# Performance work log

Hardware: AMD Instinct MI355X
Metric: run time of the kernel (lower is better)

The kernel has to match this reference:

```python
import jax, jax.numpy as jnp
import numpy as np

VOCAB = 256
UNITS = 512

def setup_inputs() -> dict:
    key = jax.random.key(0)
    ks = jax.random.split(key, 7)
    B, T = 64, 1024
    scale = 0.02
    return {
        "inputs": jax.random.randint(ks[0], (B, T), 0, VOCAB, dtype=jnp.int32),
        "emb": jax.random.normal(ks[1], (VOCAB, VOCAB), dtype=jnp.float32) * scale,
        "Wx": jax.random.normal(ks[2], (VOCAB, UNITS), dtype=jnp.float32) * scale,
        "Wh": jax.random.normal(ks[3], (UNITS, UNITS), dtype=jnp.float32) * scale,
        "b": jnp.zeros((UNITS,), dtype=jnp.float32),
        "Wd": jax.random.normal(ks[4], (UNITS, VOCAB), dtype=jnp.float32) * scale,
        "bd": jnp.zeros((VOCAB,), dtype=jnp.float32),
    }

def reference(inputs, emb, Wx, Wh, b, Wd, bd):
    # Embedding lookup: [B, T] -> [B, T, VOCAB]
    x = emb[inputs]
    B = x.shape[0]
    # Precompute input projection for all timesteps (one big GEMM)
    xp = jnp.einsum("bte,eu->btu", x, Wx) + b  # [B, T, U]
    h0 = jnp.zeros((B, Wh.shape[0]), dtype=x.dtype)

    def step(h, xp_t):
        h_new = jnp.tanh(xp_t + h @ Wh)  # SimpleRNN cell: tanh(x W_x + h W_h + b)
        return h_new, h_new

    _, hs = jax.lax.scan(step, h0, jnp.swapaxes(xp, 0, 1))  # hs: [T, B, U]
    hs = jnp.swapaxes(hs, 0, 1)  # [B, T, U]
    logits = jnp.einsum("btu,uv->btv", hs, Wd) + bd  # [B, T, VOCAB]
    return logits
```

## Files before the change

### kernel.cpp

```cpp
#include <hip/hip_runtime.h>
#include <math.h>

#define BB   64
#define TT_  1024
#define UU   512
#define VV   256
#define EE   256
#define TC   128

__device__ __forceinline__ float tanh_fast(float x) {
    float e = __expf(x + x);
    return 1.f - 2.f * __builtin_amdgcn_rcpf(e + 1.f);
}

__device__ __forceinline__ int swz(int a) {
    return a ^ (((a >> 3) & 7) ^ ((a >> 6) & 1));
}

__global__ __launch_bounds__(512) void e2_kernel(
    const float* __restrict__ emb, const float* __restrict__ Wx,
    const float* __restrict__ bias, float* __restrict__ E2)
{
    const int v = blockIdx.x;
    const int u = threadIdx.x;
    float acc = bias[u];
    const float* er = emb + v * EE;
    #pragma unroll 8
    for (int e = 0; e < EE; ++e)
        acc = fmaf(er[e], Wx[e * UU + u], acc);
    E2[v * UU + u] = acc;
}

__global__ __launch_bounds__(512)
void rnn_chunk_kernel(
    const int* __restrict__ toks, const float* __restrict__ E2,
    const float* __restrict__ Wh, const float* __restrict__ Wd,
    const float* __restrict__ bd,
    unsigned long long* hpub,
    float* out, int t0, int last)
{
    __shared__ __align__(16) float hstage[2][2][UU];
    __shared__ __align__(16) float xps[2][2][64];
    __shared__ int stok[2][TC];

    const int bid  = blockIdx.x;
    const int bg   = bid & 31;
    const int ug   = bid >> 5;
    const int tid  = threadIdx.x;
    const int w    = tid >> 6;
    const int lane = tid & 63;
    const int b0   = bg * 2;

    const int qsel = lane >> 5;
    const int ks   = lane & 31;
    const int quad = w * 2 + qsel;
    const int fmv  = ((ks >> 1) & 7) ^ ((ks >> 4) & 1);
    const int v0   = ug * 32 + quad * 2;

    float4 whreg[16];
    {
        const float4* Wh4 = (const float4*)Wh;
        #pragma unroll
        for (int r = 0; r < 16; ++r)
            whreg[r] = Wh4[(ks * 16 + r) * 128 + ug * 16 + quad];
    }
    #pragma unroll
    for (int r = 0; r < 16; ++r) {
        float px = whreg[r].x, py = whreg[r].y, pz = whreg[r].z, pw = whreg[r].w;
        asm volatile("" : "+v"(px), "+v"(py), "+v"(pz), "+v"(pw));
        whreg[r] = make_float4(px, py, pz, pw);
    }

    float wdreg[32];
    #pragma unroll
    for (int j = 0; j < 16; ++j) {
        const float2 wd2 = *(const float2*)(Wd + (ks * 16 + j) * VV + v0);
        wdreg[j]      = wd2.x;
        wdreg[16 + j] = wd2.y;
    }
    const float bdv0 = bd[v0];
    const float bdv1 = bd[v0 + 1];

    if (tid < 256) {
        const int b = tid >> 7, q = tid & 127;
        stok[b][q] = toks[(b0 + b) * TT_ + t0 + q];
    }
    if (tid < 128) {
        const int b = tid >> 6, u = tid & 63;
        xps[0][b][u] = E2[toks[(b0 + b) * TT_ + t0] * UU + ug * 64 + u];
    }
    __syncthreads();

    for (int tt = 0; tt < TC; ++tt) {
        const int s  = t0 + tt;
        const int sl = (s - 1) & 1;

        if (s > 0 && (w != ug || tt == 0)) {
            unsigned long long* a0 = hpub + ((size_t)sl * BB + b0) * UU + w * 64 + lane;
            unsigned long long* a1 = a0 + UU;
            volatile const unsigned long long* f0 = a0;
            volatile const unsigned long long* f1 = a1;
            const unsigned int want = (unsigned int)(s - 1);
            unsigned long long p0 = 0, p1 = 0;
            bool got = false;
            for (int it = 0; it < 24; ++it) {
                p0 = *f0; p1 = *f1;
                unsigned long long ok =
                    __ballot((unsigned int)(p0 >> 32) == want) &
                    __ballot((unsigned int)(p1 >> 32) == want);
                if (ok == 0xFFFFFFFFFFFFFFFFull) { got = true; break; }
            }
            if (!got) {
                while (true) {
                    p0 = __hip_atomic_load(a0, __ATOMIC_RELAXED, __HIP_MEMORY_SCOPE_AGENT);
                    p1 = __hip_atomic_load(a1, __ATOMIC_RELAXED, __HIP_MEMORY_SCOPE_AGENT);
                    unsigned long long ok =
                        __ballot((unsigned int)(p0 >> 32) == want) &
                        __ballot((unsigned int)(p1 >> 32) == want);
                    if (ok == 0xFFFFFFFFFFFFFFFFull) break;
                    __builtin_amdgcn_s_sleep(1);
                }
            }
            const int aa = w * 16 + (lane >> 2);
            const int fi = swz(aa) * 4 + (lane & 3);
            hstage[sl][0][fi] = __uint_as_float((unsigned int)p0);
            hstage[sl][1][fi] = __uint_as_float((unsigned int)p1);
        }
        asm volatile("s_waitcnt lgkmcnt(0)" ::: "memory");
        __builtin_amdgcn_s_barrier();

        float xpre = 0.f;
        const bool dopre = (tid < 128) && (tt + 1 < TC);
        if (dopre)
            xpre = E2[stok[tid >> 6][tt + 1] * UU + ug * 64 + (tid & 63)];

        float acc0[4] = {0.f, 0.f, 0.f, 0.f};
        float acc1[4] = {0.f, 0.f, 0.f, 0.f};
        float hsv0[16], hsv1[16];
        if (s > 0) {
            const float* H0 = hstage[sl][0];
            const float* H1 = hstage[sl][1];
            #pragma unroll
            for (int g = 0; g < 4; ++g) {
                const int as2 = (4 * ks + g) ^ fmv;
                const float4 ha = *(const float4*)(H0 + as2 * 4);
                const float4 hc = *(const float4*)(H1 + as2 * 4);
                const float av[4] = {ha.x, ha.y, ha.z, ha.w};
                const float cv[4] = {hc.x, hc.y, hc.z, hc.w};
                #pragma unroll
                for (int m = 0; m < 4; ++m) {
                    hsv0[g * 4 + m] = av[m];
                    hsv1[g * 4 + m] = cv[m];
                    const float4 wv = whreg[g * 4 + m];
                    acc0[0] = fmaf(av[m], wv.x, acc0[0]);
                    acc0[1] = fmaf(av[m], wv.y, acc0[1]);
                    acc0[2] = fmaf(av[m], wv.z, acc0[2]);
                    acc0[3] = fmaf(av[m], wv.w, acc0[3]);
                    acc1[0] = fmaf(cv[m], wv.x, acc1[0]);
                    acc1[1] = fmaf(cv[m], wv.y, acc1[1]);
                    acc1[2] = fmaf(cv[m], wv.z, acc1[2]);
                    acc1[3] = fmaf(cv[m], wv.w, acc1[3]);
                }
            }
        }
        if (dopre)
            xps[(s + 1) & 1][tid >> 6][tid & 63] = xpre;

        float tba[4];
        #pragma unroll
        for (int c = 0; c < 4; ++c) {
            const float x = (ks & 16) ? acc0[c] : acc1[c];
            const float y = __shfl_xor(x, 16, 64);
            tba[c] = ((ks & 16) ? acc1[c] : acc0[c]) + y;
        }
        float ua, ub;
        {
            const float x0 = (ks & 8) ? tba[0] : tba[2];
            const float x1 = (ks & 8) ? tba[1] : tba[3];
            const float y0 = __shfl_xor(x0, 8, 64);
            const float y1 = __shfl_xor(x1, 8, 64);
            ua = ((ks & 8) ? tba[2] : tba[0]) + y0;
            ub = ((ks & 8) ? tba[3] : tba[1]) + y1;
        }
        float v;
        {
            const float x = (ks & 4) ? ua : ub;
            const float y = __shfl_xor(x, 4, 64);
            v = ((ks & 4) ? ub : ua) + y;
        }
        v += __shfl_xor(v, 1, 64);
        v += __shfl_xor(v, 2, 64);

        if ((ks & 3) == 0) {
            const int b = (ks >> 4) & 1;
            const int c = (((ks >> 3) & 1) << 1) | ((ks >> 2) & 1);
            const int u = quad * 4 + c;
            const float h = tanh_fast(v + xps[s & 1][b][u]);
            unsigned long long* dst =
                hpub + ((size_t)(s & 1) * BB + b0 + b) * UU + ug * 64 + u;
            const unsigned long long pk =
                ((unsigned long long)(unsigned int)s << 32) | __float_as_uint(h);
            *(volatile unsigned long long*)dst = pk;
            __hip_atomic_store(dst, pk, __ATOMIC_RELAXED, __HIP_MEMORY_SCOPE_AGENT);
            hstage[s & 1][b][swz(ug * 16 + quad) * 4 + c] = h;
        }

        if (s > 0) {
            float s00 = 0.f, s01 = 0.f, s10 = 0.f, s11 = 0.f;
            #pragma unroll
            for (int g = 0; g < 4; ++g) {
                #pragma unroll
                for (int m = 0; m < 4; ++m) {
                    s00 = fmaf(hsv0[g * 4 + m], wdreg[4 * g + m],      s00);
                    s01 = fmaf(hsv0[g * 4 + m], wdreg[16 + 4 * g + m], s01);
                    s10 = fmaf(hsv1[g * 4 + m], wdreg[4 * g + m],      s10);
                    s11 = fmaf(hsv1[g * 4 + m], wdreg[16 + 4 * g + m], s11);
                }
            }
            float pa, pb;
            {
                const float x0 = (ks & 16) ? s00 : s10;
                const float x1 = (ks & 16) ? s01 : s11;
                const float y0 = __shfl_xor(x0, 16, 64);
                const float y1 = __shfl_xor(x1, 16, 64);
                pa = ((ks & 16) ? s10 : s00) + y0;
                pb = ((ks & 16) ? s11 : s01) + y1;
            }
            float L;
            {
                const float x = (ks & 8) ? pa : pb;
                const float y = __shfl_xor(x, 8, 64);
                L = ((ks & 8) ? pb : pa) + y;
            }
            L += __shfl_xor(L, 1, 64);
            L += __shfl_xor(L, 2, 64);
            L += __shfl_xor(L, 4, 64);
            if ((ks & 7) == 0) {
                const int b    = (ks >> 4) & 1;
                const int voff = (ks >> 3) & 1;
                out[((size_t)(b0 + b) * TT_ + (s - 1)) * VV + v0 + voff]
                    = L + (voff ? bdv1 : bdv0);
            }
        }
    }

    if (last) {
        const int s  = t0 + TC - 1;
        const int sl = s & 1;
        if (w != ug) {
            unsigned long long* a0 = hpub + ((size_t)sl * BB + b0) * UU + w * 64 + lane;
            unsigned long long* a1 = a0 + UU;
            volatile const unsigned long long* f0 = a0;
            volatile const unsigned long long* f1 = a1;
            const unsigned int want = (unsigned int)s;
            unsigned long long p0 = 0, p1 = 0;
            bool got = false;
            for (int it = 0; it < 24; ++it) {
                p0 = *f0; p1 = *f1;
                unsigned long long ok =
                    __ballot((unsigned int)(p0 >> 32) == want) &
                    __ballot((unsigned int)(p1 >> 32) == want);
                if (ok == 0xFFFFFFFFFFFFFFFFull) { got = true; break; }
            }
            if (!got) {
                while (true) {
                    p0 = __hip_atomic_load(a0, __ATOMIC_RELAXED, __HIP_MEMORY_SCOPE_AGENT);
                    p1 = __hip_atomic_load(a1, __ATOMIC_RELAXED, __HIP_MEMORY_SCOPE_AGENT);
                    unsigned long long ok =
                        __ballot((unsigned int)(p0 >> 32) == want) &
                        __ballot((unsigned int)(p1 >> 32) == want);
                    if (ok == 0xFFFFFFFFFFFFFFFFull) break;
                    __builtin_amdgcn_s_sleep(1);
                }
            }
            const int aa = w * 16 + (lane >> 2);
            const int fi = swz(aa) * 4 + (lane & 3);
            hstage[sl][0][fi] = __uint_as_float((unsigned int)p0);
            hstage[sl][1][fi] = __uint_as_float((unsigned int)p1);
        }
        __syncthreads();
        {
            const float* H0 = hstage[sl][0];
            const float* H1 = hstage[sl][1];
            float s00 = 0.f, s01 = 0.f, s10 = 0.f, s11 = 0.f;
            #pragma unroll
            for (int g = 0; g < 4; ++g) {
                const int as2 = (4 * ks + g) ^ fmv;
                const float4 ha = *(const float4*)(H0 + as2 * 4);
                const float4 hc = *(const float4*)(H1 + as2 * 4);
                const float av[4] = {ha.x, ha.y, ha.z, ha.w};
                const float cv[4] = {hc.x, hc.y, hc.z, hc.w};
                #pragma unroll
                for (int m = 0; m < 4; ++m) {
                    s00 = fmaf(av[m], wdreg[4 * g + m],      s00);
                    s01 = fmaf(av[m], wdreg[16 + 4 * g + m], s01);
                    s10 = fmaf(cv[m], wdreg[4 * g + m],      s10);
                    s11 = fmaf(cv[m], wdreg[16 + 4 * g + m], s11);
                }
            }
            float pa, pb;
            {
                const float x0 = (ks & 16) ? s00 : s10;
                const float x1 = (ks & 16) ? s01 : s11;
                const float y0 = __shfl_xor(x0, 16, 64);
                const float y1 = __shfl_xor(x1, 16, 64);
                pa = ((ks & 16) ? s10 : s00) + y0;
                pb = ((ks & 16) ? s11 : s01) + y1;
            }
            float L;
            {
                const float x = (ks & 8) ? pa : pb;
                const float y = __shfl_xor(x, 8, 64);
                L = ((ks & 8) ? pb : pa) + y;
            }
            L += __shfl_xor(L, 1, 64);
            L += __shfl_xor(L, 2, 64);
            L += __shfl_xor(L, 4, 64);
            if ((ks & 7) == 0) {
                const int b    = (ks >> 4) & 1;
                const int voff = (ks >> 3) & 1;
                out[((size_t)(b0 + b) * TT_ + s) * VV + v0 + voff]
                    = L + (voff ? bdv1 : bdv0);
            }
        }
    }
}

extern "C" void kernel_launch(void* const* d_in, const int* in_sizes, int n_in,
                              void* d_out, int out_size, void* d_ws, size_t ws_size,
                              hipStream_t stream)
{
    (void)in_sizes; (void)n_in; (void)ws_size; (void)out_size;

    const int*   toks = (const int*)  d_in[0];
    const float* emb  = (const float*)d_in[1];
    const float* Wx   = (const float*)d_in[2];
    const float* Wh   = (const float*)d_in[3];
    const float* bias = (const float*)d_in[4];
    const float* Wd   = (const float*)d_in[5];
    const float* bd   = (const float*)d_in[6];
    float* out = (float*)d_out;

    unsigned long long* hpub = (unsigned long long*)d_ws;
    float* E2 = (float*)(hpub + 2 * BB * UU);

    hipMemsetAsync(hpub, 0xFF, (size_t)(2 * BB * UU) * sizeof(unsigned long long), stream);
    e2_kernel<<<EE, UU, 0, stream>>>(emb, Wx, bias, E2);

    for (int c = 0; c < TT_ / TC; ++c) {
        const int t0 = c * TC;
        rnn_chunk_kernel<<<256, 512, 0, stream>>>(
            toks, E2, Wh, Wd, bd, hpub, out, t0, c == (TT_ / TC - 1));
    }
}
```

Measured before the change: 2.272 ms.

## Prefetch next-step hidden-state flags before output GEMV and double time chunk

Each wave now issues a speculative load of the next step's published hidden-state slots right after computing its own tanh outputs. The load overlaps the output-projection work, and the prefetched value is checked before falling back to polling. The time chunk per block also grows from 128 to 256, and all threads now load the token chunk. The aim is to hide cross-block polling latency on the serial recurrence and to reduce per-chunk startup overhead, at the cost of more LDS for tokens and possibly fewer parallel blocks.

Result: slower. 3.255 ms (+43.3%).

```diff
diff --git a/kernel.cpp b/kernel.cpp
--- a/kernel.cpp
+++ b/kernel.cpp
@@ -6,7 +6,7 @@
 #define UU   512
 #define VV   256
 #define EE   256
-#define TC   128
+#define TC   256
 
 __device__ __forceinline__ float tanh_fast(float x) {
     float e = __expf(x + x);
@@ -81,8 +81,8 @@
     const float bdv0 = bd[v0];
     const float bdv1 = bd[v0 + 1];
 
-    if (tid < 256) {
-        const int b = tid >> 7, q = tid & 127;
+    {
+        const int b = tid >> 8, q = tid & (TC - 1);
         stok[b][q] = toks[(b0 + b) * TT_ + t0 + q];
     }
     if (tid < 128) {
@@ -90,6 +90,9 @@
         xps[0][b][u] = E2[toks[(b0 + b) * TT_ + t0] * UU + ug * 64 + u];
     }
     __syncthreads();
+
+    unsigned long long q0 = 0, q1 = 0;
+    bool pre = false;
 
     for (int tt = 0; tt < TC; ++tt) {
         const int s  = t0 + tt;
@@ -103,21 +106,27 @@
             const unsigned int want = (unsigned int)(s - 1);
             unsigned long long p0 = 0, p1 = 0;
             bool got = false;
-            for (int it = 0; it < 24; ++it) {
-                p0 = *f0; p1 = *f1;
-                unsigned long long ok =
-                    __ballot((unsigned int)(p0 >> 32) == want) &
-                    __ballot((unsigned int)(p1 >> 32) == want);
-                if (ok == 0xFFFFFFFFFFFFFFFFull) { got = true; break; }
+            if (pre) {
+                p0 = q0; p1 = q1;
+                got = (__ballot(((unsigned int)(p0 >> 32) == want) &&
+                                ((unsigned int)(p1 >> 32) == want))
+                       == 0xFFFFFFFFFFFFFFFFull);
+            }
+            if (!got) {
+                for (int it = 0; it < 24; ++it) {
+                    p0 = *f0; p1 = *f1;
+                    if (__ballot(((unsigned int)(p0 >> 32) == want) &&
+                                 ((unsigned int)(p1 >> 32) == want))
+                        == 0xFFFFFFFFFFFFFFFFull) { got = true; break; }
+                }
             }
             if (!got) {
                 while (true) {
                     p0 = __hip_atomic_load(a0, __ATOMIC_RELAXED, __HIP_MEMORY_SCOPE_AGENT);
                     p1 = __hip_atomic_load(a1, __ATOMIC_RELAXED, __HIP_MEMORY_SCOPE_AGENT);
-                    unsigned long long ok =
-                        __ballot((unsigned int)(p0 >> 32) == want) &
-                        __ballot((unsigned int)(p1 >> 32) == want);
-                    if (ok == 0xFFFFFFFFFFFFFFFFull) break;
+                    if (__ballot(((unsigned int)(p0 >> 32) == want) &&
+                                 ((unsigned int)(p1 >> 32) == want))
+                        == 0xFFFFFFFFFFFFFFFFull) break;
                     __builtin_amdgcn_s_sleep(1);
                 }
             }
@@ -126,6 +135,7 @@
             hstage[sl][0][fi] = __uint_as_float((unsigned int)p0);
             hstage[sl][1][fi] = __uint_as_float((unsigned int)p1);
         }
+        pre = false;
         asm volatile("s_waitcnt lgkmcnt(0)" ::: "memory");
         __builtin_amdgcn_s_barrier();
 
@@ -205,6 +215,14 @@
             hstage[s & 1][b][swz(ug * 16 + quad) * 4 + c] = h;
         }
 
+        if (w != ug && (tt + 1 < TC || last)) {
+            unsigned long long* n0 =
+                hpub + ((size_t)(s & 1) * BB + b0) * UU + w * 64 + lane;
+            q0 = *(volatile const unsigned long long*)n0;
+            q1 = *(volatile const unsigned long long*)(n0 + UU);
+            pre = true;
+        }
+
         if (s > 0) {
             float s00 = 0.f, s01 = 0.f, s10 = 0.f, s11 = 0.f;
             #pragma unroll
@@ -255,21 +273,27 @@
             const unsigned int want = (unsigned int)s;
             unsigned long long p0 = 0, p1 = 0;
             bool got = false;
-            for (int it = 0; it < 24; ++it) {
-                p0 = *f0; p1 = *f1;
-                unsigned long long ok =
-                    __ballot((unsigned int)(p0 >> 32) == want) &
-                    __ballot((unsigned int)(p1 >> 32) == want);
-                if (ok == 0xFFFFFFFFFFFFFFFFull) { got = true; break; }
+            if (pre) {
+                p0 = q0; p1 = q1;
+                got = (__ballot(((unsigned int)(p0 >> 32) == want) &&
+                                ((unsigned int)(p1 >> 32) == want))
+                       == 0xFFFFFFFFFFFFFFFFull);
+            }
+            if (!got) {
+                for (int it = 0; it < 24; ++it) {
+                    p0 = *f0; p1 = *f1;
+                    if (__ballot(((unsigned int)(p0 >> 32) == want) &&
+                                 ((unsigned int)(p1 >> 32) == want))
+                        == 0xFFFFFFFFFFFFFFFFull) { got = true; break; }
+                }
             }
             if (!got) {
                 while (true) {
                     p0 = __hip_atomic_load(a0, __ATOMIC_RELAXED, __HIP_MEMORY_SCOPE_AGENT);
                     p1 = __hip_atomic_load(a1, __ATOMIC_RELAXED, __HIP_MEMORY_SCOPE_AGENT);
-                    unsigned long long ok =
-                        __ballot((unsigned int)(p0 >> 32) == want) &
-                        __ballot((unsigned int)(p1 >> 32) == want);
-                    if (ok == 0xFFFFFFFFFFFFFFFFull) break;
+                    if (__ballot(((unsigned int)(p0 >> 32) == want) &&
+                                 ((unsigned int)(p1 >> 32) == want))
+                        == 0xFFFFFFFFFFFFFFFFull) break;
                     __builtin_amdgcn_s_sleep(1);
                 }
             }
```
